# Kernel optimization log

Measured on AMD Instinct MI355X. Metric: run time of the kernel, lower is better.

The kernel has to match this reference:

```python
import jax, jax.numpy as jnp
import numpy as np

B, N, F = 8, 2048, 256

def setup_inputs() -> dict:
    key = jax.random.key(0)
    ks = jax.random.split(key, 8)
    X = jax.random.normal(ks[0], (B, N, F), dtype=jnp.float32)
    A_geo = jax.random.uniform(ks[1], (N, N), dtype=jnp.float32)
    distance_matrix = jax.random.uniform(ks[2], (N, N), dtype=jnp.float32)
    W_w = jax.random.normal(ks[3], (F, F), dtype=jnp.float32) * 0.05
    W_b = jax.random.normal(ks[4], (F,), dtype=jnp.float32) * 0.05
    a1 = jax.random.normal(ks[5], (F,), dtype=jnp.float32) * 0.05  # attn_fc weight, first half (for h_i)
    a2 = jax.random.normal(ks[6], (F,), dtype=jnp.float32) * 0.05  # attn_fc weight, second half (for h_j)
    attn_b = jax.random.normal(ks[7], (1,), dtype=jnp.float32) * 0.05
    threshold = jnp.ones((1,), dtype=jnp.float32) * 0.3
    return {"X": X, "A_geo": A_geo, "distance_matrix": distance_matrix,
            "W_w": W_w, "W_b": W_b, "a1": a1, "a2": a2,
            "attn_b": attn_b, "threshold": threshold}

def reference(X, A_geo, distance_matrix, W_w, W_b, a1, a2, attn_b, threshold):
    alpha = 0.1  # leaky relu slope
    h = jnp.einsum('bnf,of->bno', X, W_w) + W_b            # (B,N,F)
    # attn_fc(cat(h_i,h_j)) == h_i@a1 + h_j@a2 + b (linear decomposition of concat)
    s1 = jnp.einsum('bnf,f->bn', h, a1)                    # score contribution of h_i
    s2 = jnp.einsum('bnf,f->bn', h, a2)                    # score contribution of h_j
    e = jax.nn.leaky_relu(s1[:, :, None] + s2[:, None, :] + attn_b[0],
                          negative_slope=alpha)            # (B,N,N)
    n = distance_matrix.shape[0]
    idx = jnp.arange(n)
    D = distance_matrix.at[idx, idx].set(1.0)              # fill_diagonal_(1.0)
    e = e + 1.0 / (D + 1e-5)[None, :, :]
    mask = jax.nn.sigmoid(10.0 * (A_geo - threshold[0]))   # (N,N)
    e = e * mask[None, :, :]
    attention = jax.nn.softmax(e, axis=-1)                 # dropout: eval mode (identity)
    h_prime = jnp.einsum('bnm,bmf->bnf', attention, h)
    return h_prime
```

## Files before the change

kernel.cpp:

```cpp
#include <hip/hip_runtime.h>
#include <hip/hip_bf16.h>
#include <math.h>

#define Bsz 8
#define Nn  2048
#define Ff  256
#define KCAP 1024
#define THR 60.0f

typedef short short8 __attribute__((ext_vector_type(8)));
typedef float f32x4  __attribute__((ext_vector_type(4)));
typedef unsigned short u16x4 __attribute__((ext_vector_type(4)));
typedef unsigned short u16x8 __attribute__((ext_vector_type(8)));
typedef unsigned int uint;

static __device__ __forceinline__ unsigned short f2bf(float v) {
    __hip_bfloat16 b = __float2bfloat16(v);
    return *reinterpret_cast<unsigned short*>(&b);
}
static __device__ __forceinline__ float bf2f(unsigned short u) {
    return __uint_as_float((uint)u << 16);
}
static __device__ __forceinline__ float fast_rcp(float x) {
    return __builtin_amdgcn_rcpf(x);
}

__global__ __launch_bounds__(512) void k_h(const float* __restrict__ X,
                                           const float* __restrict__ W,
                                           const float* __restrict__ Wb,
                                           const float* __restrict__ a1,
                                           const float* __restrict__ a2,
                                           unsigned short* __restrict__ h,
                                           float* __restrict__ s1,
                                           float* __restrict__ s2) {
    __shared__ char smem[45056];
    char* w_lds = smem;
    char* x_lds = smem + 32768;
    float (*sred1)[4][16] = (float(*)[4][16])(smem + 40960);
    float (*sred2)[4][16] = (float(*)[4][16])(smem + 40960 + 2048);

    const int tid  = threadIdx.x;
    const int lane = tid & 63;
    const int w    = tid >> 6;
    const int r0   = blockIdx.x * 64;
    const int b    = r0 >> 11;
    const int n0   = r0 & 2047;

    f32x4 acc[2][4];
#pragma unroll
    for (int mt = 0; mt < 2; mt++)
#pragma unroll
        for (int nt = 0; nt < 4; nt++) acc[mt][nt] = (f32x4)0.f;

    float4 wv[8], xv[2];
    auto gload = [&](int kc) {
        const int f0 = kc * 64;
#pragma unroll
        for (int p = 0; p < 8; p++) {
            int idx = tid + p * 512;
            int o = idx >> 4, fi = idx & 15;
            wv[p] = *(const float4*)&W[(size_t)o * Ff + f0 + fi * 4];
        }
#pragma unroll
        for (int p = 0; p < 2; p++) {
            int idx = tid + p * 512;
            int n = idx >> 4, fi = idx & 15;
            xv[p] = *(const float4*)&X[(size_t)(r0 + n) * Ff + f0 + fi * 4];
        }
    };
    auto swrite = [&]() {
#pragma unroll
        for (int p = 0; p < 8; p++) {
            int idx = tid + p * 512;
            int o = idx >> 4, fi = idx & 15;
            u16x4 pk = {f2bf(wv[p].x), f2bf(wv[p].y), f2bf(wv[p].z), f2bf(wv[p].w)};
            *(u16x4*)(w_lds + ((o * 128 + fi * 8) ^ ((o & 7) << 4))) = pk;
        }
#pragma unroll
        for (int p = 0; p < 2; p++) {
            int idx = tid + p * 512;
            int n = idx >> 4, fi = idx & 15;
            u16x4 pk = {f2bf(xv[p].x), f2bf(xv[p].y), f2bf(xv[p].z), f2bf(xv[p].w)};
            *(u16x4*)(x_lds + ((n * 128 + fi * 8) ^ ((n & 7) << 4))) = pk;
        }
    };

    gload(0);
    for (int kc = 0; kc < 4; kc++) {
        __syncthreads();
        swrite();
        __syncthreads();
        if (kc < 3) gload(kc + 1);
#pragma unroll
        for (int kt = 0; kt < 2; kt++) {
            short8 bfr[4];
#pragma unroll
            for (int nt = 0; nt < 4; nt++) {
                int n = nt * 16 + (lane & 15);
                bfr[nt] = *(const short8*)(x_lds + ((n * 128 + kt * 64 + (lane >> 4) * 16) ^ ((n & 7) << 4)));
            }
#pragma unroll
            for (int mt = 0; mt < 2; mt++) {
                int o = w * 32 + mt * 16 + (lane & 15);
                short8 afr = *(const short8*)(w_lds + ((o * 128 + kt * 64 + (lane >> 4) * 16) ^ ((o & 7) << 4)));
#pragma unroll
                for (int nt = 0; nt < 4; nt++)
                    acc[mt][nt] = __builtin_amdgcn_mfma_f32_16x16x32_bf16(afr, bfr[nt], acc[mt][nt], 0, 0, 0);
            }
        }
    }

    __syncthreads();
    float s1p[4] = {0.f, 0.f, 0.f, 0.f};
    float s2p[4] = {0.f, 0.f, 0.f, 0.f};
#pragma unroll
    for (int mt = 0; mt < 2; mt++) {
#pragma unroll
        for (int reg = 0; reg < 4; reg++) {
            int o = w * 32 + mt * 16 + (lane >> 4) * 4 + reg;
            float wb = Wb[o], a1v = a1[o], a2v = a2[o];
#pragma unroll
            for (int nt = 0; nt < 4; nt++) {
                float hv = acc[mt][nt][reg] + wb;
                int nl = nt * 16 + (lane & 15);
                *(unsigned short*)(w_lds + nl * 512 + ((o * 2) ^ ((nl & 7) << 4))) = f2bf(hv);
                s1p[nt] += hv * a1v;
                s2p[nt] += hv * a2v;
            }
        }
    }
#pragma unroll
    for (int nt = 0; nt < 4; nt++) {
        s1p[nt] += __shfl_xor(s1p[nt], 16); s1p[nt] += __shfl_xor(s1p[nt], 32);
        s2p[nt] += __shfl_xor(s2p[nt], 16); s2p[nt] += __shfl_xor(s2p[nt], 32);
    }
    if (lane < 16) {
#pragma unroll
        for (int nt = 0; nt < 4; nt++) { sred1[w][nt][lane] = s1p[nt]; sred2[w][nt][lane] = s2p[nt]; }
    }
    __syncthreads();

#pragma unroll
    for (int p = 0; p < 4; p++) {
        int id = tid + p * 512;
        int nl = id >> 5;
        int c16 = (id & 31) * 16;
        u16x8 v = *(const u16x8*)(w_lds + nl * 512 + (c16 ^ ((nl & 7) << 4)));
        *(u16x8*)&h[((size_t)(b * Nn + n0 + nl)) * Ff + (id & 31) * 8] = v;
    }
    if (tid < 64) {
        int nt = tid >> 4, col = tid & 15;
        float v = 0.f;
#pragma unroll
        for (int k = 0; k < 8; k++) v += sred1[k][nt][col];
        s1[b * Nn + n0 + nt * 16 + col] = v;
    } else if (tid < 128) {
        int t2 = tid - 64;
        int nt = t2 >> 4, col = t2 & 15;
        float v = 0.f;
#pragma unroll
        for (int k = 0; k < 8; k++) v += sred2[k][nt][col];
        s2[b * Nn + n0 + nt * 16 + col] = v;
    }
}

__global__ __launch_bounds__(256) void k_attn(const unsigned short* __restrict__ h,
                                              const float* __restrict__ s1,
                                              const float* __restrict__ s2,
                                              const float* __restrict__ Ageo,
                                              const float* __restrict__ Dm,
                                              const float* __restrict__ ab_p,
                                              const float* __restrict__ thr_p,
                                              float* __restrict__ out) {
    __shared__ uint  ejs[KCAP];
    __shared__ float emks[KCAP];
    __shared__ float edgs[KCAP];
    __shared__ float red[4];
    __shared__ uint  cptr;

    const int i    = blockIdx.x;
    const int tid  = threadIdx.x;
    const int lane = tid & 63;
    const int w    = tid >> 6;
    const float c10 = 10.0f * thr_p[0];

    if (tid == 0) cptr = 0;
    const int j0 = tid * 8;
    float4 a0 = *(const float4*)&Ageo[(size_t)i * Nn + j0];
    float4 a1v = *(const float4*)&Ageo[(size_t)i * Nn + j0 + 4];
    float4 d0 = *(const float4*)&Dm[(size_t)i * Nn + j0];
    float4 d1 = *(const float4*)&Dm[(size_t)i * Nn + j0 + 4];
    float av[8] = {a0.x, a0.y, a0.z, a0.w, a1v.x, a1v.y, a1v.z, a1v.w};
    float dv[8] = {d0.x, d0.y, d0.z, d0.w, d1.x, d1.y, d1.z, d1.w};
    float mk[8], gg[8];
    float m = 0.0f;
#pragma unroll
    for (int c = 0; c < 8; c++) {
        float dd = (j0 + c == i) ? 1.0f : dv[c];
        float mkv = fast_rcp(1.0f + __expf(c10 - 10.0f * av[c]));
        float g   = mkv * fast_rcp(dd + 1e-5f);
        mk[c] = mkv;
        gg[c] = g;
        m = fmaxf(m, g);
    }
#pragma unroll
    for (int dd = 32; dd; dd >>= 1) m = fmaxf(m, __shfl_xor(m, dd));
    if (lane == 0) red[w] = m;
    __syncthreads();
    float gmax = fmaxf(fmaxf(red[0], red[1]), fmaxf(red[2], red[3]));
    const float cut = gmax - THR;
#pragma unroll
    for (int c = 0; c < 8; c++) {
        if (gg[c] > cut) {
            uint slot = atomicAdd(&cptr, 1u);
            if (slot < KCAP) {
                ejs[slot]  = (uint)(j0 + c);
                emks[slot] = mk[c];
                edgs[slot] = gg[c] - gmax;
            }
        }
    }
    __syncthreads();
    const int C = min(cptr, (uint)KCAP);

    const int b0 = w, b1 = w + 4;
    const float ab = ab_p[0];
    const float s1v0 = s1[b0 * Nn + i] + ab;
    const float s1v1 = s1[b1 * Nn + i] + ab;
    const float* s2b0 = s2 + b0 * Nn;
    const float* s2b1 = s2 + b1 * Nn;
    const unsigned short* h0 = h + (size_t)b0 * Nn * Ff;
    const unsigned short* h1 = h + (size_t)b1 * Nn * Ff;

    float4 acc0 = make_float4(0.f, 0.f, 0.f, 0.f);
    float4 acc1 = make_float4(0.f, 0.f, 0.f, 0.f);
    float ps0 = 0.f, ps1 = 0.f;

    uint  jA  = ejs[0];
    float mkA = emks[0];
    float dgA = edgs[0];
    float s2A0 = s2b0[jA], s2A1 = s2b1[jA];
    ushort4 hvA0 = *(const ushort4*)&h0[(size_t)jA * Ff + lane * 4];
    ushort4 hvA1 = *(const ushort4*)&h1[(size_t)jA * Ff + lane * 4];

    for (int c = 0; c < C; c++) {
        int cn = (c + 1 < C) ? c + 1 : c;
        uint  jB  = ejs[cn];
        float mkB = emks[cn];
        float dgB = edgs[cn];
        float s2B0 = s2b0[jB], s2B1 = s2b1[jB];
        ushort4 hvB0 = *(const ushort4*)&h0[(size_t)jB * Ff + lane * 4];
        ushort4 hvB1 = *(const ushort4*)&h1[(size_t)jB * Ff + lane * 4];

        float sa = s1v0 + s2A0;
        sa = sa > 0.f ? sa : 0.1f * sa;
        float p0 = __expf(sa * mkA + dgA);
        ps0 += p0;
        acc0.x += p0 * bf2f(hvA0.x);
        acc0.y += p0 * bf2f(hvA0.y);
        acc0.z += p0 * bf2f(hvA0.z);
        acc0.w += p0 * bf2f(hvA0.w);

        float sb = s1v1 + s2A1;
        sb = sb > 0.f ? sb : 0.1f * sb;
        float p1 = __expf(sb * mkA + dgA);
        ps1 += p1;
        acc1.x += p1 * bf2f(hvA1.x);
        acc1.y += p1 * bf2f(hvA1.y);
        acc1.z += p1 * bf2f(hvA1.z);
        acc1.w += p1 * bf2f(hvA1.w);

        jA = jB; mkA = mkB; dgA = dgB;
        s2A0 = s2B0; s2A1 = s2B1; hvA0 = hvB0; hvA1 = hvB1;
    }

    float inv0 = 1.0f / ps0;
    float inv1 = 1.0f / ps1;
    *(float4*)&out[((size_t)(b0 * Nn + i)) * Ff + lane * 4] =
        make_float4(acc0.x * inv0, acc0.y * inv0, acc0.z * inv0, acc0.w * inv0);
    *(float4*)&out[((size_t)(b1 * Nn + i)) * Ff + lane * 4] =
        make_float4(acc1.x * inv1, acc1.y * inv1, acc1.z * inv1, acc1.w * inv1);
}

extern "C" void kernel_launch(void* const* d_in, const int* in_sizes, int n_in,
                              void* d_out, int out_size, void* d_ws, size_t ws_size,
                              hipStream_t stream) {
    const float* X    = (const float*)d_in[0];
    const float* Ageo = (const float*)d_in[1];
    const float* Dm   = (const float*)d_in[2];
    const float* Ww   = (const float*)d_in[3];
    const float* Wb   = (const float*)d_in[4];
    const float* a1   = (const float*)d_in[5];
    const float* a2   = (const float*)d_in[6];
    const float* ab   = (const float*)d_in[7];
    const float* thr  = (const float*)d_in[8];
    float* out = (float*)d_out;

    char* ws = (char*)d_ws;
    float* s1 = (float*)ws;
    float* s2 = s1 + (size_t)Bsz * Nn;
    unsigned short* h = (unsigned short*)(s2 + (size_t)Bsz * Nn);

    k_h<<<256, 512, 0, stream>>>(X, Ww, Wb, a1, a2, h, s1, s2);
    k_attn<<<Nn, 256, 0, stream>>>(h, s1, s2, Ageo, Dm, ab, thr, out);
}
```

Before: 26.92 us.

## Split sparse-list construction into separate kernel writing compacted entries to global

Moves the mask/distance scan and candidate compaction out of the attention kernel into a new kernel, k_sl, that writes packed (j, mask, logit offset) uint4 entries and per-row counts to workspace. The gather kernel then only streams these entries, which removes the LDS arrays and the barrier from its prologue and makes each entry a single vector load. The candidate capacity is also halved to 512. The change adds a memset, an extra kernel launch and a global round trip for the entries. The smaller cap may silently truncate rows that have more surviving candidates.

```diff
diff --git a/kernel.cpp b/kernel.cpp
--- a/kernel.cpp
+++ b/kernel.cpp
@@ -5,7 +5,7 @@
 #define Bsz 8
 #define Nn  2048
 #define Ff  256
-#define KCAP 1024
+#define KCAP 512
 #define THR 60.0f
 
 typedef short short8 __attribute__((ext_vector_type(8)));
@@ -23,6 +23,54 @@
 }
 static __device__ __forceinline__ float fast_rcp(float x) {
     return __builtin_amdgcn_rcpf(x);
+}
+
+__global__ __launch_bounds__(256) void k_sl(const float* __restrict__ Ageo,
+                                            const float* __restrict__ Dm,
+                                            const float* __restrict__ thr_p,
+                                            uint4* __restrict__ ent,
+                                            uint* __restrict__ cnt) {
+    __shared__ float red[4];
+    const int i    = blockIdx.x;
+    const int tid  = threadIdx.x;
+    const int lane = tid & 63;
+    const int w    = tid >> 6;
+    const float c10 = 10.0f * thr_p[0];
+
+    const int j0 = tid * 8;
+    float4 a0 = *(const float4*)&Ageo[(size_t)i * Nn + j0];
+    float4 a1v = *(const float4*)&Ageo[(size_t)i * Nn + j0 + 4];
+    float4 d0 = *(const float4*)&Dm[(size_t)i * Nn + j0];
+    float4 d1 = *(const float4*)&Dm[(size_t)i * Nn + j0 + 4];
+    float av[8] = {a0.x, a0.y, a0.z, a0.w, a1v.x, a1v.y, a1v.z, a1v.w};
+    float dv[8] = {d0.x, d0.y, d0.z, d0.w, d1.x, d1.y, d1.z, d1.w};
+    float mk[8], gg[8];
+    float m = 0.0f;
+#pragma unroll
+    for (int c = 0; c < 8; c++) {
+        float dd = (j0 + c == i) ? 1.0f : dv[c];
+        float mkv = fast_rcp(1.0f + __expf(c10 - 10.0f * av[c]));
+        float g   = mkv * fast_rcp(dd + 1e-5f);
+        mk[c] = mkv;
+        gg[c] = g;
+        m = fmaxf(m, g);
+    }
+#pragma unroll
+    for (int dd = 32; dd; dd >>= 1) m = fmaxf(m, __shfl_xor(m, dd));
+    if (lane == 0) red[w] = m;
+    __syncthreads();
+    const float gmax = fmaxf(fmaxf(red[0], red[1]), fmaxf(red[2], red[3]));
+    const float cut = gmax - THR;
+#pragma unroll
+    for (int c = 0; c < 8; c++) {
+        if (gg[c] > cut) {
+            uint slot = atomicAdd(&cnt[i], 1u);
+            if (slot < KCAP)
+                ent[(size_t)i * KCAP + slot] =
+                    make_uint4((uint)(j0 + c), __float_as_uint(mk[c]),
+                               __float_as_uint(gg[c] - gmax), 0u);
+        }
+    }
 }
 
 __global__ __launch_bounds__(512) void k_h(const float* __restrict__ X,
@@ -164,64 +212,18 @@
     }
 }
 
-__global__ __launch_bounds__(256) void k_attn(const unsigned short* __restrict__ h,
-                                              const float* __restrict__ s1,
-                                              const float* __restrict__ s2,
-                                              const float* __restrict__ Ageo,
-                                              const float* __restrict__ Dm,
-                                              const float* __restrict__ ab_p,
-                                              const float* __restrict__ thr_p,
-                                              float* __restrict__ out) {
-    __shared__ uint  ejs[KCAP];
-    __shared__ float emks[KCAP];
-    __shared__ float edgs[KCAP];
-    __shared__ float red[4];
-    __shared__ uint  cptr;
-
+__global__ __launch_bounds__(256) void k_gather(const unsigned short* __restrict__ h,
+                                                const float* __restrict__ s1,
+                                                const float* __restrict__ s2,
+                                                const uint4* __restrict__ ent,
+                                                const uint* __restrict__ cnt,
+                                                const float* __restrict__ ab_p,
+                                                float* __restrict__ out) {
     const int i    = blockIdx.x;
-    const int tid  = threadIdx.x;
-    const int lane = tid & 63;
-    const int w    = tid >> 6;
-    const float c10 = 10.0f * thr_p[0];
-
-    if (tid == 0) cptr = 0;
-    const int j0 = tid * 8;
-    float4 a0 = *(const float4*)&Ageo[(size_t)i * Nn + j0];
-    float4 a1v = *(const float4*)&Ageo[(size_t)i * Nn + j0 + 4];
-    float4 d0 = *(const float4*)&Dm[(size_t)i * Nn + j0];
-    float4 d1 = *(const float4*)&Dm[(size_t)i * Nn + j0 + 4];
-    float av[8] = {a0.x, a0.y, a0.z, a0.w, a1v.x, a1v.y, a1v.z, a1v.w};
-    float dv[8] = {d0.x, d0.y, d0.z, d0.w, d1.x, d1.y, d1.z, d1.w};
-    float mk[8], gg[8];
-    float m = 0.0f;
-#pragma unroll
-    for (int c = 0; c < 8; c++) {
-        float dd = (j0 + c == i) ? 1.0f : dv[c];
-        float mkv = fast_rcp(1.0f + __expf(c10 - 10.0f * av[c]));
-        float g   = mkv * fast_rcp(dd + 1e-5f);
-        mk[c] = mkv;
-        gg[c] = g;
-        m = fmaxf(m, g);
-    }
-#pragma unroll
-    for (int dd = 32; dd; dd >>= 1) m = fmaxf(m, __shfl_xor(m, dd));
-    if (lane == 0) red[w] = m;
-    __syncthreads();
-    float gmax = fmaxf(fmaxf(red[0], red[1]), fmaxf(red[2], red[3]));
-    const float cut = gmax - THR;
-#pragma unroll
-    for (int c = 0; c < 8; c++) {
-        if (gg[c] > cut) {
-            uint slot = atomicAdd(&cptr, 1u);
-            if (slot < KCAP) {
-                ejs[slot]  = (uint)(j0 + c);
-                emks[slot] = mk[c];
-                edgs[slot] = gg[c] - gmax;
-            }
-        }
-    }
-    __syncthreads();
-    const int C = min(cptr, (uint)KCAP);
+    const int lane = threadIdx.x & 63;
+    const int w    = threadIdx.x >> 6;
+    const int C    = min(cnt[i], (uint)KCAP);
+    const uint4* el = ent + (size_t)i * KCAP;
 
     const int b0 = w, b1 = w + 4;
     const float ab = ab_p[0];
@@ -236,21 +238,20 @@
     float4 acc1 = make_float4(0.f, 0.f, 0.f, 0.f);
     float ps0 = 0.f, ps1 = 0.f;
 
-    uint  jA  = ejs[0];
-    float mkA = emks[0];
-    float dgA = edgs[0];
-    float s2A0 = s2b0[jA], s2A1 = s2b1[jA];
-    ushort4 hvA0 = *(const ushort4*)&h0[(size_t)jA * Ff + lane * 4];
-    ushort4 hvA1 = *(const ushort4*)&h1[(size_t)jA * Ff + lane * 4];
+    uint4 eA = el[0];
+    float s2A0 = s2b0[eA.x], s2A1 = s2b1[eA.x];
+    ushort4 hvA0 = *(const ushort4*)&h0[(size_t)eA.x * Ff + lane * 4];
+    ushort4 hvA1 = *(const ushort4*)&h1[(size_t)eA.x * Ff + lane * 4];
 
     for (int c = 0; c < C; c++) {
         int cn = (c + 1 < C) ? c + 1 : c;
-        uint  jB  = ejs[cn];
-        float mkB = emks[cn];
-        float dgB = edgs[cn];
-        float s2B0 = s2b0[jB], s2B1 = s2b1[jB];
-        ushort4 hvB0 = *(const ushort4*)&h0[(size_t)jB * Ff + lane * 4];
-        ushort4 hvB1 = *(const ushort4*)&h1[(size_t)jB * Ff + lane * 4];
+        uint4 eB = el[cn];
+        float s2B0 = s2b0[eB.x], s2B1 = s2b1[eB.x];
+        ushort4 hvB0 = *(const ushort4*)&h0[(size_t)eB.x * Ff + lane * 4];
+        ushort4 hvB1 = *(const ushort4*)&h1[(size_t)eB.x * Ff + lane * 4];
+
+        float mkA = __uint_as_float(eA.y);
+        float dgA = __uint_as_float(eA.z);
 
         float sa = s1v0 + s2A0;
         sa = sa > 0.f ? sa : 0.1f * sa;
@@ -270,8 +271,7 @@
         acc1.z += p1 * bf2f(hvA1.z);
         acc1.w += p1 * bf2f(hvA1.w);
 
-        jA = jB; mkA = mkB; dgA = dgB;
-        s2A0 = s2B0; s2A1 = s2B1; hvA0 = hvB0; hvA1 = hvB1;
+        eA = eB; s2A0 = s2B0; s2A1 = s2B1; hvA0 = hvB0; hvA1 = hvB1;
     }
 
     float inv0 = 1.0f / ps0;
@@ -297,10 +297,14 @@
     float* out = (float*)d_out;
 
     char* ws = (char*)d_ws;
-    float* s1 = (float*)ws;
-    float* s2 = s1 + (size_t)Bsz * Nn;
+    uint4* ent = (uint4*)ws;
+    uint*  cnt = (uint*)(ws + (size_t)Nn * KCAP * 16);
+    float* s1  = (float*)(cnt + Nn);
+    float* s2  = s1 + (size_t)Bsz * Nn;
     unsigned short* h = (unsigned short*)(s2 + (size_t)Bsz * Nn);
 
+    hipMemsetAsync(cnt, 0, Nn * sizeof(uint), stream);
+    k_sl<<<Nn, 256, 0, stream>>>(Ageo, Dm, thr, ent, cnt);
     k_h<<<256, 512, 0, stream>>>(X, Ww, Wb, a1, a2, h, s1, s2);
-    k_attn<<<Nn, 256, 0, stream>>>(h, s1, s2, Ageo, Dm, ab, thr, out);
-}
+    k_gather<<<Nn, 256, 0, stream>>>(h, s1, s2, ent, cnt, ab, out);
+}
```

After: 35.03 us. +30.1%, slower.

## Fuse projection and sparse attention into one cooperative kernel with grid sync

Applied to the files above, without the earlier changes.

Replaces the two launches with a single cooperative kernel of 512 blocks. Each wave builds the candidate list for its own row from A_geo and the distance matrix, and this work runs before a grid-wide barrier so it overlaps with the bf16 MFMA projection that the first 256 blocks compute. After the barrier, each wave computes the attention output for one row across all 8 batches. The change removes a launch and the gap between kernels, and hides the mask/candidate build behind the projection. In exchange it adds grid-sync cost, cuts the candidate cap per row to 512, gives each row less parallelism, and falls back to the old two-kernel path if the cooperative launch fails.

```diff
diff --git a/kernel.cpp b/kernel.cpp
--- a/kernel.cpp
+++ b/kernel.cpp
@@ -1,11 +1,14 @@
 #include <hip/hip_runtime.h>
 #include <hip/hip_bf16.h>
+#include <hip/hip_cooperative_groups.h>
 #include <math.h>
+
+namespace cg = cooperative_groups;
 
 #define Bsz 8
 #define Nn  2048
 #define Ff  256
-#define KCAP 1024
+#define KCAP 512
 #define THR 60.0f
 
 typedef short short8 __attribute__((ext_vector_type(8)));
@@ -23,6 +26,259 @@
 }
 static __device__ __forceinline__ float fast_rcp(float x) {
     return __builtin_amdgcn_rcpf(x);
+}
+
+__global__ __launch_bounds__(256, 2) void k_fused(const float* __restrict__ X,
+                                                  const float* __restrict__ Ageo,
+                                                  const float* __restrict__ Dm,
+                                                  const float* __restrict__ W,
+                                                  const float* __restrict__ Wb,
+                                                  const float* __restrict__ a1,
+                                                  const float* __restrict__ a2,
+                                                  const float* __restrict__ ab_p,
+                                                  const float* __restrict__ thr_p,
+                                                  unsigned short* __restrict__ h,
+                                                  float* __restrict__ s1,
+                                                  float* __restrict__ s2,
+                                                  float* __restrict__ out) {
+    __shared__ char  smem[43008];
+    __shared__ uint  ejs[4][KCAP];
+    __shared__ float emks[4][KCAP];
+    __shared__ float edgs[4][KCAP];
+    __shared__ uint  cptr[4];
+
+    const int bid  = blockIdx.x;
+    const int tid  = threadIdx.x;
+    const int lane = tid & 63;
+    const int w    = tid >> 6;
+
+    {
+        if (lane == 0) cptr[w] = 0;
+        const int i = bid * 4 + w;
+        const float c10 = 10.0f * thr_p[0];
+        float gk[32], mkk[32];
+        float m = 0.0f;
+#pragma unroll
+        for (int it = 0; it < 8; it++) {
+            int j0 = (it * 64 + lane) * 4;
+            float4 a = *(const float4*)&Ageo[(size_t)i * Nn + j0];
+            float4 d = *(const float4*)&Dm[(size_t)i * Nn + j0];
+            float av[4] = {a.x, a.y, a.z, a.w};
+            float dv[4] = {d.x, d.y, d.z, d.w};
+#pragma unroll
+            for (int c = 0; c < 4; c++) {
+                float dd = (j0 + c == i) ? 1.0f : dv[c];
+                float mkv = fast_rcp(1.0f + __expf(c10 - 10.0f * av[c]));
+                float g   = mkv * fast_rcp(dd + 1e-5f);
+                gk[it * 4 + c]  = g;
+                mkk[it * 4 + c] = mkv;
+                m = fmaxf(m, g);
+            }
+        }
+#pragma unroll
+        for (int dd2 = 32; dd2; dd2 >>= 1) m = fmaxf(m, __shfl_xor(m, dd2));
+        const float cut = m - THR;
+#pragma unroll
+        for (int k = 0; k < 32; k++) {
+            if (gk[k] > cut) {
+                uint slot = atomicAdd(&cptr[w], 1u);
+                if (slot < KCAP) {
+                    ejs[w][slot]  = (uint)((k >> 2) * 256 + lane * 4 + (k & 3));
+                    emks[w][slot] = mkk[k];
+                    edgs[w][slot] = gk[k] - m;
+                }
+            }
+        }
+    }
+
+    if (bid < 256) {
+        char* w_lds = smem;
+        char* x_lds = smem + 32768;
+        float (*sred1)[4][16] = (float(*)[4][16])(smem + 40960);
+        float (*sred2)[4][16] = (float(*)[4][16])(smem + 40960 + 1024);
+
+        const int r0 = bid * 64;
+        const int b  = r0 >> 11;
+        const int n0 = r0 & 2047;
+
+        f32x4 acc[4][4];
+#pragma unroll
+        for (int mt = 0; mt < 4; mt++)
+#pragma unroll
+            for (int nt = 0; nt < 4; nt++) acc[mt][nt] = (f32x4)0.f;
+
+        float4 wv[16], xv[4];
+        auto gload = [&](int kc) {
+            const int f0 = kc * 64;
+#pragma unroll
+            for (int p = 0; p < 16; p++) {
+                int idx = tid + p * 256;
+                int o = idx >> 4, fi = idx & 15;
+                wv[p] = *(const float4*)&W[(size_t)o * Ff + f0 + fi * 4];
+            }
+#pragma unroll
+            for (int p = 0; p < 4; p++) {
+                int idx = tid + p * 256;
+                int n = idx >> 4, fi = idx & 15;
+                xv[p] = *(const float4*)&X[(size_t)(r0 + n) * Ff + f0 + fi * 4];
+            }
+        };
+        auto swrite = [&]() {
+#pragma unroll
+            for (int p = 0; p < 16; p++) {
+                int idx = tid + p * 256;
+                int o = idx >> 4, fi = idx & 15;
+                u16x4 pk = {f2bf(wv[p].x), f2bf(wv[p].y), f2bf(wv[p].z), f2bf(wv[p].w)};
+                *(u16x4*)(w_lds + ((o * 128 + fi * 8) ^ ((o & 7) << 4))) = pk;
+            }
+#pragma unroll
+            for (int p = 0; p < 4; p++) {
+                int idx = tid + p * 256;
+                int n = idx >> 4, fi = idx & 15;
+                u16x4 pk = {f2bf(xv[p].x), f2bf(xv[p].y), f2bf(xv[p].z), f2bf(xv[p].w)};
+                *(u16x4*)(x_lds + ((n * 128 + fi * 8) ^ ((n & 7) << 4))) = pk;
+            }
+        };
+
+        gload(0);
+        for (int kc = 0; kc < 4; kc++) {
+            __syncthreads();
+            swrite();
+            __syncthreads();
+            if (kc < 3) gload(kc + 1);
+#pragma unroll
+            for (int kt = 0; kt < 2; kt++) {
+                short8 bfr[4];
+#pragma unroll
+                for (int nt = 0; nt < 4; nt++) {
+                    int n = nt * 16 + (lane & 15);
+                    bfr[nt] = *(const short8*)(x_lds + ((n * 128 + kt * 64 + (lane >> 4) * 16) ^ ((n & 7) << 4)));
+                }
+#pragma unroll
+                for (int mt = 0; mt < 4; mt++) {
+                    int o = w * 64 + mt * 16 + (lane & 15);
+                    short8 afr = *(const short8*)(w_lds + ((o * 128 + kt * 64 + (lane >> 4) * 16) ^ ((o & 7) << 4)));
+#pragma unroll
+                    for (int nt = 0; nt < 4; nt++)
+                        acc[mt][nt] = __builtin_amdgcn_mfma_f32_16x16x32_bf16(afr, bfr[nt], acc[mt][nt], 0, 0, 0);
+                }
+            }
+        }
+
+        __syncthreads();
+        float s1p[4] = {0.f, 0.f, 0.f, 0.f};
+        float s2p[4] = {0.f, 0.f, 0.f, 0.f};
+#pragma unroll
+        for (int mt = 0; mt < 4; mt++) {
+#pragma unroll
+            for (int reg = 0; reg < 4; reg++) {
+                int o = w * 64 + mt * 16 + (lane >> 4) * 4 + reg;
+                float wb = Wb[o], a1v = a1[o], a2v = a2[o];
+#pragma unroll
+                for (int nt = 0; nt < 4; nt++) {
+                    float hv = acc[mt][nt][reg] + wb;
+                    int nl = nt * 16 + (lane & 15);
+                    *(unsigned short*)(w_lds + nl * 512 + ((o * 2) ^ ((nl & 7) << 4))) = f2bf(hv);
+                    s1p[nt] += hv * a1v;
+                    s2p[nt] += hv * a2v;
+                }
+            }
+        }
+#pragma unroll
+        for (int nt = 0; nt < 4; nt++) {
+            s1p[nt] += __shfl_xor(s1p[nt], 16); s1p[nt] += __shfl_xor(s1p[nt], 32);
+            s2p[nt] += __shfl_xor(s2p[nt], 16); s2p[nt] += __shfl_xor(s2p[nt], 32);
+        }
+        if (lane < 16) {
+#pragma unroll
+            for (int nt = 0; nt < 4; nt++) { sred1[w][nt][lane] = s1p[nt]; sred2[w][nt][lane] = s2p[nt]; }
+        }
+        __syncthreads();
+
+#pragma unroll
+        for (int p = 0; p < 8; p++) {
+            int id = tid + p * 256;
+            int nl = id >> 5;
+            int c16 = (id & 31) * 16;
+            u16x8 v = *(const u16x8*)(w_lds + nl * 512 + (c16 ^ ((nl & 7) << 4)));
+            *(u16x8*)&h[((size_t)(b * Nn + n0 + nl)) * Ff + (id & 31) * 8] = v;
+        }
+        if (tid < 64) {
+            int nt = tid >> 4, col = tid & 15;
+            s1[b * Nn + n0 + nt * 16 + col] = sred1[0][nt][col] + sred1[1][nt][col] + sred1[2][nt][col] + sred1[3][nt][col];
+        } else if (tid < 128) {
+            int t2 = tid - 64;
+            int nt = t2 >> 4, col = t2 & 15;
+            s2[b * Nn + n0 + nt * 16 + col] = sred2[0][nt][col] + sred2[1][nt][col] + sred2[2][nt][col] + sred2[3][nt][col];
+        }
+    }
+
+    cg::this_grid().sync();
+
+    {
+        const int i = bid * 4 + w;
+        const int C = min((int)cptr[w], KCAP);
+        const float ab = ab_p[0];
+
+        for (int p = 0; p < 4; p++) {
+            const int b0 = p, b1 = p + 4;
+            const float s1v0 = s1[b0 * Nn + i] + ab;
+            const float s1v1 = s1[b1 * Nn + i] + ab;
+            const float* s2b0 = s2 + b0 * Nn;
+            const float* s2b1 = s2 + b1 * Nn;
+            const unsigned short* h0 = h + (size_t)b0 * Nn * Ff;
+            const unsigned short* h1 = h + (size_t)b1 * Nn * Ff;
+
+            float4 acc0 = make_float4(0.f, 0.f, 0.f, 0.f);
+            float4 acc1 = make_float4(0.f, 0.f, 0.f, 0.f);
+            float ps0 = 0.f, ps1 = 0.f;
+
+            uint  jA  = ejs[w][0];
+            float mkA = emks[w][0];
+            float dgA = edgs[w][0];
+            float s2A0 = s2b0[jA], s2A1 = s2b1[jA];
+            ushort4 hvA0 = *(const ushort4*)&h0[(size_t)jA * Ff + lane * 4];
+            ushort4 hvA1 = *(const ushort4*)&h1[(size_t)jA * Ff + lane * 4];
+
+            for (int c = 0; c < C; c++) {
+                int cn = (c + 1 < C) ? c + 1 : c;
+                uint  jB  = ejs[w][cn];
+                float mkB = emks[w][cn];
+                float dgB = edgs[w][cn];
+                float s2B0 = s2b0[jB], s2B1 = s2b1[jB];
+                ushort4 hvB0 = *(const ushort4*)&h0[(size_t)jB * Ff + lane * 4];
+                ushort4 hvB1 = *(const ushort4*)&h1[(size_t)jB * Ff + lane * 4];
+
+                float sa = s1v0 + s2A0;
+                sa = sa > 0.f ? sa : 0.1f * sa;
+                float p0 = __expf(sa * mkA + dgA);
+                ps0 += p0;
+                acc0.x += p0 * bf2f(hvA0.x);
+                acc0.y += p0 * bf2f(hvA0.y);
+                acc0.z += p0 * bf2f(hvA0.z);
+                acc0.w += p0 * bf2f(hvA0.w);
+
+                float sb = s1v1 + s2A1;
+                sb = sb > 0.f ? sb : 0.1f * sb;
+                float p1 = __expf(sb * mkA + dgA);
+                ps1 += p1;
+                acc1.x += p1 * bf2f(hvA1.x);
+                acc1.y += p1 * bf2f(hvA1.y);
+                acc1.z += p1 * bf2f(hvA1.z);
+                acc1.w += p1 * bf2f(hvA1.w);
+
+                jA = jB; mkA = mkB; dgA = dgB;
+                s2A0 = s2B0; s2A1 = s2B1; hvA0 = hvB0; hvA1 = hvB1;
+            }
+
+            float inv0 = 1.0f / ps0;
+            float inv1 = 1.0f / ps1;
+            *(float4*)&out[((size_t)(b0 * Nn + i)) * Ff + lane * 4] =
+                make_float4(acc0.x * inv0, acc0.y * inv0, acc0.z * inv0, acc0.w * inv0);
+            *(float4*)&out[((size_t)(b1 * Nn + i)) * Ff + lane * 4] =
+                make_float4(acc1.x * inv1, acc1.y * inv1, acc1.z * inv1, acc1.w * inv1);
+        }
+    }
 }
 
 __global__ __launch_bounds__(512) void k_h(const float* __restrict__ X,
@@ -172,9 +428,9 @@
                                               const float* __restrict__ ab_p,
                                               const float* __restrict__ thr_p,
                                               float* __restrict__ out) {
-    __shared__ uint  ejs[KCAP];
-    __shared__ float emks[KCAP];
-    __shared__ float edgs[KCAP];
+    __shared__ uint  ejs[2 * KCAP];
+    __shared__ float emks[2 * KCAP];
+    __shared__ float edgs[2 * KCAP];
     __shared__ float red[4];
     __shared__ uint  cptr;
 
@@ -213,7 +469,7 @@
     for (int c = 0; c < 8; c++) {
         if (gg[c] > cut) {
             uint slot = atomicAdd(&cptr, 1u);
-            if (slot < KCAP) {
+            if (slot < 2 * KCAP) {
                 ejs[slot]  = (uint)(j0 + c);
                 emks[slot] = mk[c];
                 edgs[slot] = gg[c] - gmax;
@@ -221,7 +477,7 @@
         }
     }
     __syncthreads();
-    const int C = min(cptr, (uint)KCAP);
+    const int C = min(cptr, (uint)(2 * KCAP));
 
     const int b0 = w, b1 = w + 4;
     const float ab = ab_p[0];
@@ -290,8 +546,8 @@
     const float* Dm   = (const float*)d_in[2];
     const float* Ww   = (const float*)d_in[3];
     const float* Wb   = (const float*)d_in[4];
-    const float* a1   = (const float*)d_in[5];
-    const float* a2   = (const float*)d_in[6];
+    const float* a1p  = (const float*)d_in[5];
+    const float* a2p  = (const float*)d_in[6];
     const float* ab   = (const float*)d_in[7];
     const float* thr  = (const float*)d_in[8];
     float* out = (float*)d_out;
@@ -301,6 +557,14 @@
     float* s2 = s1 + (size_t)Bsz * Nn;
     unsigned short* h = (unsigned short*)(s2 + (size_t)Bsz * Nn);
 
-    k_h<<<256, 512, 0, stream>>>(X, Ww, Wb, a1, a2, h, s1, s2);
-    k_attn<<<Nn, 256, 0, stream>>>(h, s1, s2, Ageo, Dm, ab, thr, out);
-}
+    void* args[] = {(void*)&X, (void*)&Ageo, (void*)&Dm, (void*)&Ww, (void*)&Wb,
+                    (void*)&a1p, (void*)&a2p, (void*)&ab, (void*)&thr,
+                    (void*)&h, (void*)&s1, (void*)&s2, (void*)&out};
+    hipError_t err = hipLaunchCooperativeKernel((void*)k_fused, dim3(512), dim3(256),
+                                                args, 0, stream);
+    if (err != hipSuccess) {
+        (void)hipGetLastError();
+        k_h<<<256, 512, 0, stream>>>(X, Ww, Wb, a1p, a2p, h, s1, s2);
+        k_attn<<<Nn, 256, 0, stream>>>(h, s1, s2, Ageo, Dm, ab, thr, out);
+    }
+}
```

Result: slower. 104.7 us (+288.8%).
